# Optimization experiments

Measured on AMD Instinct MI355X. Metric: run time of the kernel, lower is better.

The kernel has to match this reference:

```python
import jax, jax.numpy as jnp
import numpy as np

NEG_INF = -9e9  # matches torch code's -9000000000.0


def setup_inputs() -> dict:
    key = jax.random.key(0)
    ks = jax.random.split(key, 12)
    B, N, L = 128, 32, 36
    Ds, Dv, H = 512, 1024, 512
    span_embeddings = jax.random.normal(ks[0], (B, N, Ds), dtype=jnp.float32)
    image_embeddings = jax.random.normal(ks[1], (B, L, Dv), dtype=jnp.float32)
    span_mask = jax.random.randint(ks[2], (B, N), 0, 2).astype(jnp.float32)
    image_mask = jax.random.randint(ks[3], (B, L), 0, 2).astype(jnp.float32)
    # BilinearPairWiseClassifier weight: maps span dim -> image dim
    Wg = jax.random.normal(ks[4], (Ds, Dv), dtype=jnp.float32) / np.sqrt(Ds)
    # SimplePairWiseClassifier MLP on concat(first, second, first*second)
    W1 = jax.random.normal(ks[5], (3 * Ds, H), dtype=jnp.float32) / np.sqrt(3 * Ds)
    b1 = jnp.zeros((H,), dtype=jnp.float32)
    W2 = jax.random.normal(ks[6], (H, H), dtype=jnp.float32) / np.sqrt(H)
    b2 = jnp.zeros((H,), dtype=jnp.float32)
    W3 = jax.random.normal(ks[7], (H, 1), dtype=jnp.float32) / np.sqrt(H)
    b3 = jnp.zeros((1,), dtype=jnp.float32)
    return {
        "span_embeddings": span_embeddings,
        "image_embeddings": image_embeddings,
        "span_mask": span_mask,
        "image_mask": image_mask,
        "Wg": Wg, "W1": W1, "b1": b1, "W2": W2, "b2": b2, "W3": W3, "b3": b3,
    }


def reference(span_embeddings, image_embeddings, span_mask, image_mask,
              Wg, W1, b1, W2, b2, W3, b3):
    B, N, Ds = span_embeddings.shape
    L = image_embeddings.shape[1]

    # ---- score_grounding (vectorized B^2 loop) ----
    # mention_scores[b] = bilinear(first[b], second[b]); the off-diagonal
    # 'score' in the original loop recomputes the SAME thing (only the mask
    # varies with jdx), so one (B,N,L) tensor suffices.
    M = jnp.einsum('bnd,de,ble->bnl', span_embeddings, Wg, image_embeddings)  # (B,N,L)
    # pairwise mask over doc pairs (i uses span_mask, j uses image_mask)
    pm = span_mask[:, None, :, None] * image_mask[None, :, None, :]  # (B,B,N,L)
    pm = jnp.where(pm != 0, pm, NEG_INF)
    w = jax.nn.softmax(pm.reshape(B, B, N * L), axis=-1).reshape(B, B, N, L)
    sent_scores = jnp.einsum('inl,ijnl->ij', M, w)  # (B,B)

    # ---- score_text: all span pairs via combinations(range(N), 2) ----
    iu, ju = np.triu_indices(N, k=1)  # same order as itertools.combinations
    first = span_embeddings[:, iu]    # (B,P,Ds)
    second = span_embeddings[:, ju]   # (B,P,Ds)
    feat = jnp.concatenate([first, second, first * second], axis=-1)  # (B,P,3Ds)
    h = jax.nn.relu(feat @ W1 + b1)
    h = jax.nn.relu(h @ W2 + b2)
    text_scores = (h @ W3 + b3)[..., 0]  # (B,P)

    # ---- contrastive loss over sentence-score matrix ----
    loss = (-jnp.sum(jax.nn.log_softmax(sent_scores, axis=1))
            - jnp.sum(jax.nn.log_softmax(sent_scores.T, axis=1))) / B
    return loss, M, text_scores
```

## Files before the change

kernel.cpp:

```cpp
#include <hip/hip_runtime.h>

#define B_  128
#define N_  32
#define L_  36
#define DS  512
#define DV  1024
#define H_  512
#define P_  496
#define R_  63488
#define LSE_BLKS 128
#define FUSE_BLKS (R_ / 64)

typedef __attribute__((ext_vector_type(8))) short bf16x8;
typedef __attribute__((ext_vector_type(4))) float f32x4;

__device__ __forceinline__ ushort f2bf(float x){
  unsigned u = __builtin_bit_cast(unsigned, x);
  return (ushort)((u + 0x7FFFu + ((u >> 16) & 1u)) >> 16);
}
__device__ __forceinline__ float bf2f(ushort u){
  unsigned v = ((unsigned)u) << 16;
  return __builtin_bit_cast(float, v);
}

__device__ __forceinline__ bf16x8 pkmul(bf16x8 a, bf16x8 b){
  union { unsigned u[4]; bf16x8 v; } o;
  #pragma unroll
  for (int e = 0; e < 4; ++e){
    float p0 = bf2f((ushort)a[2*e])   * bf2f((ushort)b[2*e]);
    float p1 = bf2f((ushort)a[2*e+1]) * bf2f((ushort)b[2*e+1]);
    asm("v_cvt_pk_bf16_f32 %0, %1, %2" : "=v"(o.u[e]) : "v"(p0), "v"(p1));
  }
  return o.v;
}

__device__ __forceinline__ void gload16(const void* g, void* l){
  __builtin_amdgcn_global_load_lds((const __attribute__((address_space(1))) unsigned*)g,
                                   (__attribute__((address_space(3))) unsigned*)l, 16, 0, 0);
}

__device__ __forceinline__ float wave_sum(float v){
  #pragma unroll
  for (int m = 32; m >= 1; m >>= 1) v += __shfl_xor(v, m);
  return v;
}
__device__ __forceinline__ float wave_max(float v){
  #pragma unroll
  for (int m = 32; m >= 1; m >>= 1) v = fmaxf(v, __shfl_xor(v, m));
  return v;
}

#define SPAN_F4 524288
#define IMG_F4  1179648
#define CONV_BLKS ((SPAN_F4 + IMG_F4) / 256)
#define TR_BLKS   (512 * 5)
__global__ void prep_all(const float* __restrict__ span, const float* __restrict__ img,
                         const float* __restrict__ b3,
                         const float* __restrict__ Wg, const float* __restrict__ W1,
                         const float* __restrict__ W2,
                         const float* __restrict__ sm, const float* __restrict__ im,
                         ushort* __restrict__ spbf, ushort* __restrict__ imgbf,
                         float* __restrict__ text,
                         ushort* __restrict__ WgT, ushort* __restrict__ UVBT,
                         ushort* __restrict__ W1cT, ushort* __restrict__ W2T,
                         float* cnt_s, float* cnt_i, int* iu, int* ju, float* loss){
  __shared__ float tile[32][33];
  const int bid = blockIdx.x, tid = threadIdx.x;
  if (bid < CONV_BLKS){
    int idx = bid * 256 + tid;
    if (idx < R_) text[idx] = b3[0];
    const float* src; ushort* dst; int k;
    if (idx < SPAN_F4){ src = span; dst = spbf; k = idx; }
    else              { src = img;  dst = imgbf; k = idx - SPAN_F4; }
    float4 v = *(const float4*)&src[(size_t)k * 4];
    ushort4 o; o.x = f2bf(v.x); o.y = f2bf(v.y); o.z = f2bf(v.z); o.w = f2bf(v.w);
    *(ushort4*)&dst[(size_t)k * 4] = o;
  } else if (bid < CONV_BLKS + TR_BLKS){
    int b = bid - CONV_BLKS;
    int z = b >> 9, rem = b & 511;
    int bx = rem & 31, by = rem >> 5;
    const float* src; ushort* dst; int Nn;
    if      (z == 0){ src = Wg;            dst = WgT;            Nn = 1024; }
    else if (z == 1){ src = W1;            dst = UVBT;           Nn = 512;  }
    else if (z == 2){ src = W1 + 512*512;  dst = UVBT + 512*512; Nn = 512;  }
    else if (z == 3){ src = W1 + 1024*512; dst = W1cT;           Nn = 512;  }
    else            { src = W2;            dst = W2T;            Nn = 512;  }
    if (bx * 32 >= Nn) return;
    int n0 = bx * 32, k0 = by * 32;
    int x = tid & 31, y = tid >> 5;
    #pragma unroll
    for (int i = 0; i < 4; ++i) tile[y + 8*i][x] = src[(k0 + y + 8*i) * Nn + n0 + x];
    __syncthreads();
    if (z >= 3){
      #pragma unroll
      for (int i = 0; i < 4; ++i){
        int n = n0 + y + 8*i, k = k0 + x;
        dst[(n >> 4)*8192 + (k >> 3)*128 + (n & 15)*8 + (k & 7)] = f2bf(tile[x][y + 8*i]);
      }
    } else {
      #pragma unroll
      for (int i = 0; i < 4; ++i) dst[(n0 + y + 8*i) * 512 + k0 + x] = f2bf(tile[x][y + 8*i]);
    }
  } else {
    int t = (bid - CONV_BLKS - TR_BLKS) * 256 + tid;
    if (t < P_){
      int i = 0, rem = t, cnt = N_ - 1;
      while (rem >= cnt){ rem -= cnt; ++i; --cnt; }
      iu[t] = i; ju[t] = i + 1 + rem;
    }
    if (t < B_){
      float s = 0.f;
      for (int n = 0; n < N_; ++n) s += sm[t*N_ + n];
      cnt_s[t] = s;
    } else if (t < 2*B_){
      int j = t - B_;
      float s = 0.f;
      for (int l = 0; l < L_; ++l) s += im[j*L_ + l];
      cnt_i[j] = s;
    }
    if (t == 0) loss[0] = 0.f;
  }
}

#define S2_LDSA 8192
#define S2_BUF  24576

__global__ __launch_bounds__(512, 2) void span2_gemm(const ushort* __restrict__ A,
                                                     const ushort* __restrict__ BT2,
                                                     ushort* __restrict__ SG,
                                                     ushort* __restrict__ UV){
  __shared__ ushort lds[2 * S2_BUF];
  const int bid0 = blockIdx.x;
  const int bid = ((bid0 & 7) << 5) | (bid0 >> 3);
  const size_t m0 = (size_t)(bid & 31) * 128;
  const int ng = (bid >> 5) * 256;
  const int tid = threadIdx.x, wid = tid >> 6, lane = tid & 63;
  const int wr = wid >> 2, wc = wid & 3;
  const int quad = lane >> 4, fm = lane & 15;
  const int swz = ((fm >> 2) & 3) << 4;

  #define S2_STAGE(kt_, dst_) do {                                          \
    _Pragma("unroll")                                                       \
    for (int i_ = 0; i_ < 6; ++i_){                                         \
      int u_ = i_ * 512 + tid;                                              \
      if (u_ < 1024){                                                       \
        int row_ = u_ >> 3, ch_ = (u_ & 7) << 3;                            \
        gload16(A + (m0 + row_) * 512 + (kt_) * 64                          \
                  + (ch_ ^ (((row_ >> 2) & 3) << 4)),                       \
                (dst_) + row_ * 64 + ch_);                                  \
      } else {                                                              \
        int v_ = u_ - 1024;                                                 \
        int row_ = v_ >> 3, ch_ = (v_ & 7) << 3;                            \
        gload16(BT2 + (size_t)(ng + row_) * 512 + (kt_) * 64                \
                  + (ch_ ^ (((row_ >> 2) & 3) << 4)),                       \
                (dst_) + S2_LDSA + row_ * 64 + ch_);                        \
      }                                                                     \
    }                                                                       \
  } while (0)

  f32x4 acc[4][4] = {};
  S2_STAGE(0, lds);
  S2_STAGE(1, lds + S2_BUF);
  #pragma unroll 1
  for (int kt = 0; kt < 8; ++kt){
    if (kt < 7) asm volatile("s_waitcnt vmcnt(6)" ::: "memory");
    else        asm volatile("s_waitcnt vmcnt(0)" ::: "memory");
    __builtin_amdgcn_s_barrier();
    const ushort* bufA = lds + (kt & 1) * S2_BUF;
    const ushort* bufB = bufA + S2_LDSA;
    bf16x8 af[4][2], bg[4][2];
    #pragma unroll
    for (int m = 0; m < 4; ++m)
      #pragma unroll
      for (int kk = 0; kk < 2; ++kk)
        af[m][kk] = *(const bf16x8*)&bufA[(wr*64 + m*16 + fm) * 64
                                          + ((kk*32 + quad*8) ^ swz)];
    #pragma unroll
    for (int n = 0; n < 4; ++n)
      #pragma unroll
      for (int kk = 0; kk < 2; ++kk)
        bg[n][kk] = *(const bf16x8*)&bufB[(wc*64 + n*16 + fm) * 64
                                          + ((kk*32 + quad*8) ^ swz)];
    asm volatile("s_waitcnt lgkmcnt(0)" ::: "memory");
    __builtin_amdgcn_sched_barrier(0);
    __builtin_amdgcn_s_setprio(1);
    #pragma unroll
    for (int kk = 0; kk < 2; ++kk)
      #pragma unroll
      for (int m = 0; m < 4; ++m)
        #pragma unroll
        for (int n = 0; n < 4; ++n)
          acc[m][n] = __builtin_amdgcn_mfma_f32_16x16x32_bf16(
              af[m][kk], bg[n][kk], acc[m][n], 0, 0, 0);
    __builtin_amdgcn_s_setprio(0);
    __builtin_amdgcn_s_barrier();
    if (kt + 2 < 8) S2_STAGE(kt + 2, lds + (kt & 1) * S2_BUF);
  }
  #undef S2_STAGE

  if (ng < 1024){
    #pragma unroll
    for (int m = 0; m < 4; ++m)
      #pragma unroll
      for (int r = 0; r < 4; ++r){
        size_t row = m0 + wr*64 + m*16 + quad*4 + r;
        #pragma unroll
        for (int n = 0; n < 4; ++n){
          int col = ng + wc*64 + n*16 + fm;
          SG[row * 1024 + col] = f2bf(acc[m][n][r]);
        }
      }
  } else {
    const int ngp = ng - 1024;
    const int pcb = (ngp & 512) + (((((ngp & 511) >> 7) + (wc >> 1)) & 3) << 7)
                  + fm * 8 + (wc & 1) * 4;
    #pragma unroll
    for (int m = 0; m < 4; ++m)
      #pragma unroll
      for (int r = 0; r < 4; ++r){
        size_t row = m0 + wr*64 + m*16 + quad*4 + r;
        uint2 pk;
        asm("v_cvt_pk_bf16_f32 %0, %1, %2" : "=v"(pk.x) : "v"(acc[m][0][r]), "v"(acc[m][1][r]));
        asm("v_cvt_pk_bf16_f32 %0, %1, %2" : "=v"(pk.y) : "v"(acc[m][2][r]), "v"(acc[m][3][r]));
        *(uint2*)(UV + row * 1024 + pcb) = pk;
      }
  }
}

__global__ __launch_bounds__(256) void batched_m_mfma(const ushort* __restrict__ SGbf,
                                                      const ushort* __restrict__ imgbf,
                                                      const float* __restrict__ sm,
                                                      float* __restrict__ Mout,
                                                      float* __restrict__ Msum,
                                                      float* __restrict__ Mtot){
  const int b = blockIdx.x;
  const int tid = threadIdx.x, wid = tid >> 6, lane = tid & 63;
  const int quad = lane >> 4, fm = lane & 15;
  __shared__ float red[4][32][48];
  __shared__ float shr[4];
  f32x4 acc[2][3] = {};
  const int wk = wid * 256;
  const ushort* Ab = SGbf + (size_t)b * 32 * 1024;
  const ushort* Bb = imgbf + (size_t)b * 36 * 1024;
  #pragma unroll
  for (int ks = 0; ks < 8; ++ks){
    const int k = wk + ks * 32 + quad * 8;
    bf16x8 af[2], bg[3];
    af[0] = *(const bf16x8*)&Ab[(0*16 + fm) * 1024 + k];
    af[1] = *(const bf16x8*)&Ab[(1*16 + fm) * 1024 + k];
    bg[0] = *(const bf16x8*)&Bb[(0*16 + fm) * 1024 + k];
    bg[1] = *(const bf16x8*)&Bb[(1*16 + fm) * 1024 + k];
    bg[2] = *(const bf16x8*)&Bb[(2*16 + fm) * 1024 + k];
    #pragma unroll
    for (int i = 0; i < 2; ++i)
      #pragma unroll
      for (int j = 0; j < 3; ++j)
        acc[i][j] = __builtin_amdgcn_mfma_f32_16x16x32_bf16(af[i], bg[j], acc[i][j], 0, 0, 0);
  }
  #pragma unroll
  for (int i = 0; i < 2; ++i)
    #pragma unroll
    for (int j = 0; j < 3; ++j)
      #pragma unroll
      for (int r = 0; r < 4; ++r)
        red[wid][i*16 + quad*4 + r][j*16 + fm] = acc[i][j][r];
  __syncthreads();
  float tot = 0.f;
  #pragma unroll
  for (int q = 0; q < 5; ++q){
    int out = tid + 256 * q;
    if (out < N_*L_){
      int n = out / L_, l = out - n * L_;
      float v = red[0][n][l] + red[1][n][l] + red[2][n][l] + red[3][n][l];
      Mout[b * (N_*L_) + out] = v;
      tot += v;
    }
  }
  tot = wave_sum(tot);
  if (lane == 0) shr[wid] = tot;
  __syncthreads();
  if (tid == 0) Mtot[b] = shr[0] + shr[1] + shr[2] + shr[3];
  if (tid < L_){
    float s = 0.f;
    for (int n = 0; n < N_; ++n){
      float mv = red[0][n][tid] + red[1][n][tid] + red[2][n][tid] + red[3][n][tid];
      s += mv * sm[b*N_ + n];
    }
    Msum[b*L_ + tid] = s;
  }
}

__device__ void lse_loss_body(const float* __restrict__ Msum, const float* __restrict__ im,
                              const float* __restrict__ cnt_s, const float* __restrict__ cnt_i,
                              const float* __restrict__ Mtot, float* __restrict__ out,
                              int i, float* sh ){
  const int tid = threadIdx.x;
  const int t = tid & 127;
  const int w4 = tid >> 6, lane = tid & 63;
  float sr = 0.f, sc = 0.f;
  #pragma unroll 4
  for (int l = 0; l < L_; ++l){
    sr += Msum[i*L_ + l] * im[t*L_ + l];
    sc += Msum[t*L_ + l] * im[i*L_ + l];
  }
  const float dr = cnt_s[i] * cnt_i[t];
  const float vr = (dr != 0.f) ? (sr / dr) : (Mtot[i] * (1.f/(float)(N_*L_)));
  const float dc = cnt_s[t] * cnt_i[i];
  const float vc = (dc != 0.f) ? (sc / dc) : (Mtot[t] * (1.f/(float)(N_*L_)));

  float m = wave_max(vr);
  if (lane == 0) sh[w4] = m;
  __syncthreads();
  const float mr = fmaxf(sh[0], sh[1]);
  __syncthreads();
  float e = wave_sum(expf(vr - mr));
  if (lane == 0) sh[w4] = e;
  __syncthreads();
  const float ser = sh[0] + sh[1];
  __syncthreads();
  float rs = wave_sum(vr);
  if (lane == 0) sh[w4] = rs;
  __syncthreads();
  const float rst = sh[0] + sh[1];
  __syncthreads();
  float mc0 = wave_max(vc);
  if (lane == 0) sh[w4] = mc0;
  __syncthreads();
  const float mc = fmaxf(sh[0], sh[1]);
  __syncthreads();
  float ec = wave_sum(expf(vc - mc));
  if (lane == 0) sh[w4] = ec;
  __syncthreads();
  const float sec = sh[0] + sh[1];
  if (tid == 0){
    float contrib = (mr + logf(ser)) + (mc + logf(sec)) - 2.f * rst / (float)B_;
    atomicAdd(out, contrib);
  }
}

__global__ __launch_bounds__(256, 2) void gemm_fused(
    const ushort* __restrict__ spbf, const ushort* __restrict__ W1cT,
    const ushort* __restrict__ W2T, const ushort* __restrict__ UV,
    const float* __restrict__ b1, const float* __restrict__ b2,
    const float* __restrict__ W3, const float* __restrict__ b3,
    const int* __restrict__ iu, const int* __restrict__ ju,
    float* __restrict__ text,
    const float* __restrict__ Msum, const float* __restrict__ im,
    const float* __restrict__ cnt_s, const float* __restrict__ cnt_i,
    const float* __restrict__ Mtot, float* __restrict__ loss){
  __shared__ ushort panel[32768];
  __shared__ float  partial[4][64];

  if (blockIdx.x < LSE_BLKS){
    lse_loss_body(Msum, im, cnt_s, cnt_i, Mtot, loss, blockIdx.x, (float*)partial);
    return;
  }
  const size_t m0 = (size_t)(blockIdx.x - LSE_BLKS) * 64;
  const int tid = threadIdx.x, wid = tid >> 6, lane = tid & 63;
  const int wc = wid;
  const int quad = lane >> 4, fm = lane & 15;
  const int f7 = fm & 7;

  {
    int row = tid >> 2;
    int c0  = tid & 3;
    int row_g = (int)m0 + row;
    int b = row_g / P_, p = row_g - b * P_;
    const ushort* xr = spbf + (size_t)(b * N_ + iu[p]) * 512;
    const ushort* yr = spbf + (size_t)(b * N_ + ju[p]) * 512;
    ushort* pr = panel + row * 512;
    int r7 = row & 7;
    #pragma unroll
    for (int i = 0; i < 16; ++i){
      int ch = c0 + 4*i;
      bf16x8 x = *(const bf16x8*)&xr[ch*8];
      bf16x8 y = *(const bf16x8*)&yr[ch*8];
      *(bf16x8*)&pr[(ch ^ r7) * 8] = pkmul(x, y);
    }
  }
  const ushort* pB1 = W1cT + wc * 65536 + quad * 128 + fm * 8;
  const ushort* pB2 = W2T  + wc * 65536 + quad * 128 + fm * 8;
  const int ar0 = (0*16 + fm) * 512;
  const int ar1 = (1*16 + fm) * 512;
  const int ar2 = (2*16 + fm) * 512;
  const int ar3 = (3*16 + fm) * 512;

  __syncthreads();

  #define LOADB(P, D, kt_) {                                                    \
    _Pragma("unroll")                                                           \
    for (int n_ = 0; n_ < 8; ++n_)                                              \
      D[n_] = *(const bf16x8*)&(P)[n_ * 8192 + (kt_) * 512];                    \
  }
  #define ITER(AC, kt_, CUR, NXT, P) {                                          \
    if ((kt_) < 15) LOADB(P, NXT, (kt_) + 1);                                   \
    int c_ = ((((kt_) * 4 + quad) ^ f7) * 8);                                   \
    bf16x8 a0 = *(const bf16x8*)&panel[ar0 + c_];                               \
    bf16x8 a1 = *(const bf16x8*)&panel[ar1 + c_];                               \
    bf16x8 a2 = *(const bf16x8*)&panel[ar2 + c_];                               \
    bf16x8 a3 = *(const bf16x8*)&panel[ar3 + c_];                               \
    __builtin_amdgcn_s_setprio(1);                                              \
    _Pragma("unroll")                                                           \
    for (int n_ = 0; n_ < 8; ++n_){                                             \
      AC[0][n_] = __builtin_amdgcn_mfma_f32_16x16x32_bf16(a0, CUR[n_], AC[0][n_], 0, 0, 0); \
      AC[1][n_] = __builtin_amdgcn_mfma_f32_16x16x32_bf16(a1, CUR[n_], AC[1][n_], 0, 0, 0); \
      AC[2][n_] = __builtin_amdgcn_mfma_f32_16x16x32_bf16(a2, CUR[n_], AC[2][n_], 0, 0, 0); \
      AC[3][n_] = __builtin_amdgcn_mfma_f32_16x16x32_bf16(a3, CUR[n_], AC[3][n_], 0, 0, 0); \
    }                                                                           \
    __builtin_amdgcn_s_setprio(0);                                              \
  }

  f32x4 acc[4][8] = {};
  bf16x8 g0[8], g1[8];
  LOADB(pB1, g0, 0);
  #pragma unroll 1
  for (int it = 0; it < 8; ++it){
    ITER(acc, 2*it,     g0, g1, pB1);
    ITER(acc, 2*it + 1, g1, g0, pB1);
  }
  __syncthreads();
  LOADB(pB2, g0, 0);

  {
    float b1v[8];
    #pragma unroll
    for (int n = 0; n < 8; ++n) b1v[n] = b1[wc*128 + n*16 + fm];
    const int uvoff = wc*128 + fm*8;
    #pragma unroll
    for (int m = 0; m < 4; ++m)
      #pragma unroll
      for (int r = 0; r < 4; ++r){
        int rowL = m*16 + quad*4 + r;
        int row_g = (int)m0 + rowL;
        int b = row_g / P_, p = row_g - b * P_;
        bf16x8 uv8 = *(const bf16x8*)(UV + (size_t)(b * N_ + iu[p]) * 1024 + uvoff);
        bf16x8 vv8 = *(const bf16x8*)(UV + (size_t)(b * N_ + ju[p]) * 1024 + 512 + uvoff);
        ushort* pr = panel + rowL * 512;
        int r7 = rowL & 7;
        #pragma unroll
        for (int n = 0; n < 8; n += 2){
          float h0 = fmaxf(acc[m][n][r]   + bf2f((ushort)uv8[n])   + bf2f((ushort)vv8[n])   + b1v[n],   0.f);
          float h1 = fmaxf(acc[m][n+1][r] + bf2f((ushort)uv8[n+1]) + bf2f((ushort)vv8[n+1]) + b1v[n+1], 0.f);
          unsigned pk;
          asm("v_cvt_pk_bf16_f32 %0, %1, %2" : "=v"(pk) : "v"(h0), "v"(h1));
          int col0 = wc*128 + n*16 + fm;
          int col1 = col0 + 16;
          pr[((((col0 >> 3) ^ r7) << 3) + (col0 & 7))] = (ushort)pk;
          pr[((((col1 >> 3) ^ r7) << 3) + (col1 & 7))] = (ushort)(pk >> 16);
        }
      }
  }
  __syncthreads();

  f32x4 acc2[4][8] = {};
  #pragma unroll 1
  for (int it = 0; it < 8; ++it){
    ITER(acc2, 2*it,     g0, g1, pB2);
    ITER(acc2, 2*it + 1, g1, g0, pB2);
  }
  #undef ITER
  #undef LOADB

  {
    float w3v[8], b2v[8];
    #pragma unroll
    for (int n = 0; n < 8; ++n){
      int col = wc*128 + n*16 + fm;
      w3v[n] = W3[col]; b2v[n] = b2[col];
    }
    #pragma unroll
    for (int m = 0; m < 4; ++m)
      #pragma unroll
      for (int r = 0; r < 4; ++r){
        float s = 0.f;
        #pragma unroll
        for (int n = 0; n < 8; ++n){
          float h = fmaxf(acc2[m][n][r] + b2v[n], 0.f);
          s = fmaf(h, w3v[n], s);
        }
        s += __shfl_xor(s, 1); s += __shfl_xor(s, 2);
        s += __shfl_xor(s, 4); s += __shfl_xor(s, 8);
        if (fm == 0) partial[wc][m*16 + quad*4 + r] = s;
      }
  }
  __syncthreads();
  if (tid < 64)
    text[m0 + tid] = partial[0][tid] + partial[1][tid] + partial[2][tid]
                   + partial[3][tid] + b3[0];
}

extern "C" void kernel_launch(void* const* d_in, const int* in_sizes, int n_in,
                              void* d_out, int out_size, void* d_ws, size_t ws_size,
                              hipStream_t stream) {
  const float* span = (const float*)d_in[0];
  const float* img  = (const float*)d_in[1];
  const float* sm   = (const float*)d_in[2];
  const float* im   = (const float*)d_in[3];
  const float* Wg   = (const float*)d_in[4];
  const float* W1   = (const float*)d_in[5];
  const float* b1   = (const float*)d_in[6];
  const float* W2   = (const float*)d_in[7];
  const float* b2   = (const float*)d_in[8];
  const float* W3   = (const float*)d_in[9];
  const float* b3   = (const float*)d_in[10];

  float* out  = (float*)d_out;
  float* loss = out;
  float* Mout = out + 1;
  float* text = out + 1 + B_*N_*L_;

  ushort* wsu  = (ushort*)d_ws;
  ushort* Zbf  = wsu;
  ushort* h1bf = Zbf + (size_t)R_*512;
  ushort* UVbf = h1bf + (size_t)R_*512;
  ushort* SGbf = UVbf + (size_t)4096*1024;
  ushort* spbf = SGbf + (size_t)4096*1024;
  ushort* imgbf= spbf + 4096*512;
  ushort* BT2  = imgbf + (size_t)(B_*L_ + 12)*1024;
  ushort* WgT  = BT2;
  ushort* UVBT = BT2 + 1024*512;
  ushort* W1cT = UVBT + 1024*512;
  ushort* W2T  = W1cT + 512*512;
  float* Msum  = (float*)(W2T + 512*512);
  float* Mtot  = Msum + B_*L_;
  float* cnt_s = Mtot + B_;
  float* cnt_i = cnt_s + B_;
  int*   iu    = (int*)(cnt_i + B_);
  int*   ju    = iu + P_;

  prep_all<<<CONV_BLKS + TR_BLKS + 2, 256, 0, stream>>>(
      span, img, b3, Wg, W1, W2, sm, im,
      spbf, imgbf, text, WgT, UVBT, W1cT, W2T, cnt_s, cnt_i, iu, ju, loss);

  span2_gemm<<<256, 512, 0, stream>>>(spbf, BT2, SGbf, UVbf);

  batched_m_mfma<<<B_, 256, 0, stream>>>(SGbf, imgbf, sm, Mout, Msum, Mtot);

  gemm_fused<<<LSE_BLKS + FUSE_BLKS, 256, 0, stream>>>(
      spbf, W1cT, W2T, UVbf, b1, b2, W3, b3, iu, ju, text,
      Msum, im, cnt_s, cnt_i, Mtot, loss);
}
```

Before: 190.1 us.

## Enlarge fused MLP GEMM tile to 128 rows with 8 waves per block

The fused pair-MLP GEMM now processes 128 rows per block with 512 threads. Each of the 8 waves owns a 64-column slice and all 128 rows, so every weight fragment loaded from global memory feeds twice as many MFMAs. The UV read offsets are remapped to the permuted UV column layout. The batched M kernel also moves to 8 waves splitting K more finely. The cost is a 128KB LDS panel per block, which caps occupancy at one block per CU, and fewer blocks in the grid.

```diff
diff --git a/kernel.cpp b/kernel.cpp
--- a/kernel.cpp
+++ b/kernel.cpp
@@ -9,7 +9,7 @@
 #define P_  496
 #define R_  63488
 #define LSE_BLKS 128
-#define FUSE_BLKS (R_ / 64)
+#define FUSE_BLKS (R_ / 128)
 
 typedef __attribute__((ext_vector_type(8))) short bf16x8;
 typedef __attribute__((ext_vector_type(4))) float f32x4;
@@ -227,7 +227,7 @@
   }
 }
 
-__global__ __launch_bounds__(256) void batched_m_mfma(const ushort* __restrict__ SGbf,
+__global__ __launch_bounds__(512) void batched_m_mfma(const ushort* __restrict__ SGbf,
                                                       const ushort* __restrict__ imgbf,
                                                       const float* __restrict__ sm,
                                                       float* __restrict__ Mout,
@@ -236,14 +236,14 @@
   const int b = blockIdx.x;
   const int tid = threadIdx.x, wid = tid >> 6, lane = tid & 63;
   const int quad = lane >> 4, fm = lane & 15;
-  __shared__ float red[4][32][48];
-  __shared__ float shr[4];
+  __shared__ float red[8][32][48];
+  __shared__ float shr[8];
   f32x4 acc[2][3] = {};
-  const int wk = wid * 256;
+  const int wk = wid * 128;
   const ushort* Ab = SGbf + (size_t)b * 32 * 1024;
   const ushort* Bb = imgbf + (size_t)b * 36 * 1024;
   #pragma unroll
-  for (int ks = 0; ks < 8; ++ks){
+  for (int ks = 0; ks < 4; ++ks){
     const int k = wk + ks * 32 + quad * 8;
     bf16x8 af[2], bg[3];
     af[0] = *(const bf16x8*)&Ab[(0*16 + fm) * 1024 + k];
@@ -267,11 +267,13 @@
   __syncthreads();
   float tot = 0.f;
   #pragma unroll
-  for (int q = 0; q < 5; ++q){
-    int out = tid + 256 * q;
+  for (int q = 0; q < 3; ++q){
+    int out = tid + 512 * q;
     if (out < N_*L_){
       int n = out / L_, l = out - n * L_;
-      float v = red[0][n][l] + red[1][n][l] + red[2][n][l] + red[3][n][l];
+      float v = 0.f;
+      #pragma unroll
+      for (int w = 0; w < 8; ++w) v += red[w][n][l];
       Mout[b * (N_*L_) + out] = v;
       tot += v;
     }
@@ -279,11 +281,18 @@
   tot = wave_sum(tot);
   if (lane == 0) shr[wid] = tot;
   __syncthreads();
-  if (tid == 0) Mtot[b] = shr[0] + shr[1] + shr[2] + shr[3];
+  if (tid == 0){
+    float s = 0.f;
+    #pragma unroll
+    for (int w = 0; w < 8; ++w) s += shr[w];
+    Mtot[b] = s;
+  }
   if (tid < L_){
     float s = 0.f;
     for (int n = 0; n < N_; ++n){
-      float mv = red[0][n][tid] + red[1][n][tid] + red[2][n][tid] + red[3][n][tid];
+      float mv = 0.f;
+      #pragma unroll
+      for (int w = 0; w < 8; ++w) mv += red[w][n][tid];
       s += mv * sm[b*N_ + n];
     }
     Msum[b*L_ + tid] = s;
@@ -338,7 +347,7 @@
   }
 }
 
-__global__ __launch_bounds__(256, 2) void gemm_fused(
+__global__ __launch_bounds__(512, 2) void gemm_fused(
     const ushort* __restrict__ spbf, const ushort* __restrict__ W1cT,
     const ushort* __restrict__ W2T, const ushort* __restrict__ UV,
     const float* __restrict__ b1, const float* __restrict__ b2,
@@ -348,14 +357,14 @@
     const float* __restrict__ Msum, const float* __restrict__ im,
     const float* __restrict__ cnt_s, const float* __restrict__ cnt_i,
     const float* __restrict__ Mtot, float* __restrict__ loss){
-  __shared__ ushort panel[32768];
-  __shared__ float  partial[4][64];
+  __shared__ ushort panel[65536];
+  __shared__ float  partial[8][128];
 
   if (blockIdx.x < LSE_BLKS){
     lse_loss_body(Msum, im, cnt_s, cnt_i, Mtot, loss, blockIdx.x, (float*)partial);
     return;
   }
-  const size_t m0 = (size_t)(blockIdx.x - LSE_BLKS) * 64;
+  const size_t m0 = (size_t)(blockIdx.x - LSE_BLKS) * 128;
   const int tid = threadIdx.x, wid = tid >> 6, lane = tid & 63;
   const int wc = wid;
   const int quad = lane >> 4, fm = lane & 15;
@@ -378,40 +387,35 @@
       *(bf16x8*)&pr[(ch ^ r7) * 8] = pkmul(x, y);
     }
   }
-  const ushort* pB1 = W1cT + wc * 65536 + quad * 128 + fm * 8;
-  const ushort* pB2 = W2T  + wc * 65536 + quad * 128 + fm * 8;
-  const int ar0 = (0*16 + fm) * 512;
-  const int ar1 = (1*16 + fm) * 512;
-  const int ar2 = (2*16 + fm) * 512;
-  const int ar3 = (3*16 + fm) * 512;
+  const ushort* pB1 = W1cT + wc * 32768 + quad * 128 + fm * 8;
+  const ushort* pB2 = W2T  + wc * 32768 + quad * 128 + fm * 8;
 
   __syncthreads();
 
   #define LOADB(P, D, kt_) {                                                    \
     _Pragma("unroll")                                                           \
-    for (int n_ = 0; n_ < 8; ++n_)                                              \
+    for (int n_ = 0; n_ < 4; ++n_)                                              \
       D[n_] = *(const bf16x8*)&(P)[n_ * 8192 + (kt_) * 512];                    \
   }
   #define ITER(AC, kt_, CUR, NXT, P) {                                          \
     if ((kt_) < 15) LOADB(P, NXT, (kt_) + 1);                                   \
     int c_ = ((((kt_) * 4 + quad) ^ f7) * 8);                                   \
-    bf16x8 a0 = *(const bf16x8*)&panel[ar0 + c_];                               \
-    bf16x8 a1 = *(const bf16x8*)&panel[ar1 + c_];                               \
-    bf16x8 a2 = *(const bf16x8*)&panel[ar2 + c_];                               \
-    bf16x8 a3 = *(const bf16x8*)&panel[ar3 + c_];                               \
+    bf16x8 a_[8];                                                               \
+    _Pragma("unroll")                                                           \
+    for (int m_ = 0; m_ < 8; ++m_)                                              \
+      a_[m_] = *(const bf16x8*)&panel[(m_*16 + fm) * 512 + c_];                 \
     __builtin_amdgcn_s_setprio(1);                                              \
     _Pragma("unroll")                                                           \
-    for (int n_ = 0; n_ < 8; ++n_){                                             \
-      AC[0][n_] = __builtin_amdgcn_mfma_f32_16x16x32_bf16(a0, CUR[n_], AC[0][n_], 0, 0, 0); \
-      AC[1][n_] = __builtin_amdgcn_mfma_f32_16x16x32_bf16(a1, CUR[n_], AC[1][n_], 0, 0, 0); \
-      AC[2][n_] = __builtin_amdgcn_mfma_f32_16x16x32_bf16(a2, CUR[n_], AC[2][n_], 0, 0, 0); \
-      AC[3][n_] = __builtin_amdgcn_mfma_f32_16x16x32_bf16(a3, CUR[n_], AC[3][n_], 0, 0, 0); \
-    }                                                                           \
+    for (int m_ = 0; m_ < 8; ++m_)                                              \
+      _Pragma("unroll")                                                         \
+      for (int n_ = 0; n_ < 4; ++n_)                                            \
+        AC[m_][n_] = __builtin_amdgcn_mfma_f32_16x16x32_bf16(                   \
+            a_[m_], CUR[n_], AC[m_][n_], 0, 0, 0);                              \
     __builtin_amdgcn_s_setprio(0);                                              \
   }
 
-  f32x4 acc[4][8] = {};
-  bf16x8 g0[8], g1[8];
+  f32x4 acc[8][4] = {};
+  bf16x8 g0[4], g1[4];
   LOADB(pB1, g0, 0);
   #pragma unroll 1
   for (int it = 0; it < 8; ++it){
@@ -422,28 +426,29 @@
   LOADB(pB2, g0, 0);
 
   {
-    float b1v[8];
-    #pragma unroll
-    for (int n = 0; n < 8; ++n) b1v[n] = b1[wc*128 + n*16 + fm];
-    const int uvoff = wc*128 + fm*8;
-    #pragma unroll
-    for (int m = 0; m < 4; ++m)
+    float b1v[4];
+    #pragma unroll
+    for (int n = 0; n < 4; ++n) b1v[n] = b1[wc*64 + n*16 + fm];
+    const int uvoff = ((wc >> 1) & 3) * 128 + fm * 8 + (wc & 1) * 4;
+    #pragma unroll
+    for (int m = 0; m < 8; ++m)
       #pragma unroll
       for (int r = 0; r < 4; ++r){
         int rowL = m*16 + quad*4 + r;
         int row_g = (int)m0 + rowL;
         int b = row_g / P_, p = row_g - b * P_;
-        bf16x8 uv8 = *(const bf16x8*)(UV + (size_t)(b * N_ + iu[p]) * 1024 + uvoff);
-        bf16x8 vv8 = *(const bf16x8*)(UV + (size_t)(b * N_ + ju[p]) * 1024 + 512 + uvoff);
+        union { uint2 u; ushort s[4]; } uv, vv;
+        uv.u = *(const uint2*)(UV + (size_t)(b * N_ + iu[p]) * 1024 + uvoff);
+        vv.u = *(const uint2*)(UV + (size_t)(b * N_ + ju[p]) * 1024 + 512 + uvoff);
         ushort* pr = panel + rowL * 512;
         int r7 = rowL & 7;
         #pragma unroll
-        for (int n = 0; n < 8; n += 2){
-          float h0 = fmaxf(acc[m][n][r]   + bf2f((ushort)uv8[n])   + bf2f((ushort)vv8[n])   + b1v[n],   0.f);
-          float h1 = fmaxf(acc[m][n+1][r] + bf2f((ushort)uv8[n+1]) + bf2f((ushort)vv8[n+1]) + b1v[n+1], 0.f);
+        for (int n = 0; n < 4; n += 2){
+          float h0 = fmaxf(acc[m][n][r]   + bf2f(uv.s[n])   + bf2f(vv.s[n])   + b1v[n],   0.f);
+          float h1 = fmaxf(acc[m][n+1][r] + bf2f(uv.s[n+1]) + bf2f(vv.s[n+1]) + b1v[n+1], 0.f);
           unsigned pk;
           asm("v_cvt_pk_bf16_f32 %0, %1, %2" : "=v"(pk) : "v"(h0), "v"(h1));
-          int col0 = wc*128 + n*16 + fm;
+          int col0 = wc*64 + n*16 + fm;
           int col1 = col0 + 16;
           pr[((((col0 >> 3) ^ r7) << 3) + (col0 & 7))] = (ushort)pk;
           pr[((((col1 >> 3) ^ r7) << 3) + (col1 & 7))] = (ushort)(pk >> 16);
@@ -452,7 +457,7 @@
   }
   __syncthreads();
 
-  f32x4 acc2[4][8] = {};
+  f32x4 acc2[8][4] = {};
   #pragma unroll 1
   for (int it = 0; it < 8; ++it){
     ITER(acc2, 2*it,     g0, g1, pB2);
@@ -462,19 +467,19 @@
   #undef LOADB
 
   {
-    float w3v[8], b2v[8];
-    #pragma unroll
-    for (int n = 0; n < 8; ++n){
-      int col = wc*128 + n*16 + fm;
+    float w3v[4], b2v[4];
+    #pragma unroll
+    for (int n = 0; n < 4; ++n){
+      int col = wc*64 + n*16 + fm;
       w3v[n] = W3[col]; b2v[n] = b2[col];
     }
     #pragma unroll
-    for (int m = 0; m < 4; ++m)
+    for (int m = 0; m < 8; ++m)
       #pragma unroll
       for (int r = 0; r < 4; ++r){
         float s = 0.f;
         #pragma unroll
-        for (int n = 0; n < 8; ++n){
+        for (int n = 0; n < 4; ++n){
           float h = fmaxf(acc2[m][n][r] + b2v[n], 0.f);
           s = fmaf(h, w3v[n], s);
         }
@@ -484,9 +489,12 @@
       }
   }
   __syncthreads();
-  if (tid < 64)
-    text[m0 + tid] = partial[0][tid] + partial[1][tid] + partial[2][tid]
-                   + partial[3][tid] + b3[0];
+  if (tid < 128){
+    float s = b3[0];
+    #pragma unroll
+    for (int w = 0; w < 8; ++w) s += partial[w][tid];
+    text[m0 + tid] = s;
+  }
 }
 
 extern "C" void kernel_launch(void* const* d_in, const int* in_sizes, int n_in,
@@ -534,9 +542,9 @@
 
   span2_gemm<<<256, 512, 0, stream>>>(spbf, BT2, SGbf, UVbf);
 
-  batched_m_mfma<<<B_, 256, 0, stream>>>(SGbf, imgbf, sm, Mout, Msum, Mtot);
-
-  gemm_fused<<<LSE_BLKS + FUSE_BLKS, 256, 0, stream>>>(
+  batched_m_mfma<<<B_, 512, 0, stream>>>(SGbf, imgbf, sm, Mout, Msum, Mtot);
+
+  gemm_fused<<<LSE_BLKS + FUSE_BLKS, 512, 0, stream>>>(
       spbf, W1cT, W2T, UVbf, b1, b2, W3, b3, iu, ju, text,
       Msum, im, cnt_s, cnt_i, Mtot, loss);
 }
```

Result: slower. 198.6 us (+4.4%).
